# Kernel tuning notes

Hardware: AMD Instinct MI355X
Metric: run time of the kernel (lower is better)

The kernel has to match this reference:

```python
import jax, jax.numpy as jnp
import numpy as np

S, B, T, D, TS, V = 256, 8, 1024, 512, 512, 32000
LN_EPS = 1e-5


def setup_inputs() -> dict:
    key = jax.random.key(0)
    ks = jax.random.split(key, 16)
    std = 0.02
    inp = {
        "outs": jax.random.normal(ks[0], (S, B, D), jnp.float32),
        "graph_state": jax.random.normal(ks[1], (T, B, D), jnp.float32),
        "graph_padding_mask": jnp.zeros((B, T), bool),
        "copy_seq": jax.random.randint(ks[2], (T, B), 0, V),
        # single-head attention projections
        "Wq": std * jax.random.normal(ks[3], (D, D), jnp.float32),
        "bq": jnp.zeros((D,), jnp.float32),
        "Wk": std * jax.random.normal(ks[4], (D, D), jnp.float32),
        "bk": jnp.zeros((D,), jnp.float32),
        "Wv": std * jax.random.normal(ks[5], (D, D), jnp.float32),
        "bv": jnp.zeros((D,), jnp.float32),
        "Wo": std * jax.random.normal(ks[6], (D, D), jnp.float32),
        "bo": jnp.zeros((D,), jnp.float32),
        # layer norm
        "ln_g": jnp.ones((D,), jnp.float32),
        "ln_b": jnp.zeros((D,), jnp.float32),
        # transfer / generator / diverter linears
        "Wt": std * jax.random.normal(ks[7], (TS, D), jnp.float32),
        "bt": jnp.zeros((TS,), jnp.float32),
        "Wgen": std * jax.random.normal(ks[8], (V, TS), jnp.float32),
        "bgen": jnp.zeros((V,), jnp.float32),
        "Wdiv": std * jax.random.normal(ks[9], (2, TS), jnp.float32),
        "bdiv": jnp.zeros((2,), jnp.float32),
    }
    return inp


def _layer_norm(x, g, b):
    mu = jnp.mean(x, -1, keepdims=True)
    var = jnp.mean(jnp.square(x - mu), -1, keepdims=True)
    return (x - mu) * jax.lax.rsqrt(var + LN_EPS) * g + b


def reference(outs, graph_state, graph_padding_mask, copy_seq,
              Wq, bq, Wk, bk, Wv, bv, Wo, bo, ln_g, ln_b,
              Wt, bt, Wgen, bgen, Wdiv, bdiv):
    scale = 1.0 / jnp.sqrt(jnp.asarray(D, outs.dtype))
    q = (outs @ Wq.T + bq) * scale              # [S,B,D]
    k = graph_state @ Wk.T + bk                 # [T,B,D]
    v = graph_state @ Wv.T + bv                 # [T,B,D]
    scores = jnp.einsum("sbd,tbd->sbt", q, k)   # [S,B,T]
    scores = jnp.where(graph_padding_mask[None, :, :], -1e9, scores)
    attn = jax.nn.softmax(scores, axis=-1)      # alignment_weight [S,B,T]
    ctx = jnp.einsum("sbt,tbd->sbd", attn, v)
    x = ctx @ Wo.T + bo
    outs = _layer_norm(outs + x, ln_g, ln_b)
    outs_token = jnp.tanh(outs @ Wt.T + bt)     # [S,B,TS]
    gates = jax.nn.softmax(outs_token @ Wdiv.T + bdiv, axis=-1)
    gen_gate, copy_gate = gates[..., 0:1], gates[..., 1:2]
    probs = gen_gate * jax.nn.softmax(outs_token @ Wgen.T + bgen, axis=-1)  # [S,B,V]
    # copy indices: [T,B] -> [S,B,T] broadcast (indices < V, so no vocab extension)
    index = jnp.broadcast_to(copy_seq.T[None, :, :], (S, B, T))
    copy_probs = copy_gate * attn               # [S,B,T]
    s_idx = jnp.arange(S)[:, None, None]
    b_idx = jnp.arange(B)[None, :, None]
    probs = probs.at[s_idx, b_idx, index].add(copy_probs)
    ll = jnp.log(probs + 1e-12)
    return ll
```

## Files before the change

kernel.cpp:

```cpp
#include <hip/hip_runtime.h>
#include <hip/hip_bf16.h>
#include <math.h>

#define SS 256
#define BB 8
#define TT 1024
#define DD 512
#define TSD 512
#define VV 32000
#define LN_EPS_F 1e-5f
#define VHALF 16000

typedef __attribute__((ext_vector_type(8))) short bf16x8;
typedef __attribute__((ext_vector_type(4))) float f32x4;

__device__ __forceinline__ unsigned short f2bf(float f) {
    union { float f; unsigned int u; } c; c.f = f;
    unsigned int u = c.u;
    return (unsigned short)((u + 0x7fffu + ((u >> 16) & 1u)) >> 16);
}
__device__ __forceinline__ float bf2f(unsigned short s) {
    union { unsigned int u; float f; } c; c.u = ((unsigned int)s) << 16;
    return c.f;
}

__device__ __forceinline__ void glls16(const void* g, void* l) {
    __builtin_amdgcn_global_load_lds(
        (const __attribute__((address_space(1))) unsigned int*)g,
        (__attribute__((address_space(3))) unsigned int*)l,
        16, 0, 0);
}

__device__ __forceinline__ float warp_red_sum(float v) {
    for (int o = 32; o > 0; o >>= 1) v += __shfl_down(v, o, 64);
    return v;
}
__device__ __forceinline__ float warp_red_max(float v) {
    for (int o = 32; o > 0; o >>= 1) v = fmaxf(v, __shfl_down(v, o, 64));
    return v;
}
__device__ __forceinline__ float block_red_sum(float v, float* s) {
    int lane = threadIdx.x & 63, wid = threadIdx.x >> 6;
    v = warp_red_sum(v);
    __syncthreads();
    if (lane == 0) s[wid] = v;
    __syncthreads();
    float r = 0.f;
    int nw = blockDim.x >> 6;
    for (int i = 0; i < nw; i++) r += s[i];
    return r;
}
__device__ __forceinline__ float block_red_max(float v, float* s) {
    int lane = threadIdx.x & 63, wid = threadIdx.x >> 6;
    v = warp_red_max(v);
    __syncthreads();
    if (lane == 0) s[wid] = v;
    __syncthreads();
    float r = s[0];
    int nw = blockDim.x >> 6;
    for (int i = 1; i < nw; i++) r = fmaxf(r, s[i]);
    return r;
}

template<int IN_BF16, int OUT_BF16, int ACT, int SWZ>
__global__ __launch_bounds__(256) void mfma_gemm(
    const void* __restrict__ Ap, long long lda, long long aoff,
    const void* __restrict__ Bp, long long ldb, long long boff,
    const float* __restrict__ bias,
    void* __restrict__ Cp, long long ldc, long long coff,
    int K, float scale, float* __restrict__ rsum)
{
    __shared__ __align__(16) unsigned short smem[2 * 128 * 64];
    unsigned short* As = smem;
    unsigned short* Bs = smem + 128 * 64;
    const int tid = threadIdx.x;
    const int lane = tid & 63;
    const int wave = tid >> 6;
    const int wm = (wave >> 1) << 6;
    const int wn = (wave & 1) << 6;
    const int lane15 = lane & 15;
    const int quad = lane >> 4;

    int bx = blockIdx.x, by = blockIdx.y;
    if (SWZ) {
        unsigned int nx = gridDim.x;
        unsigned int nwg = nx * gridDim.y;
        unsigned int lin = blockIdx.y * nx + blockIdx.x;
        unsigned int q = nwg >> 3, r = nwg & 7u;
        unsigned int xcd = lin & 7u, loc = lin >> 3;
        unsigned int wg = (xcd < r ? xcd * (q + 1u) : r * (q + 1u) + (xcd - r) * q) + loc;
        bx = (int)(wg % nx);
        by = (int)(wg / nx);
    }
    const long long m0 = (long long)bx * 128;
    const long long n0 = (long long)by * 128;
    const long long z = blockIdx.z;

    f32x4 acc[4][4];
#pragma unroll
    for (int i = 0; i < 4; i++)
#pragma unroll
        for (int j = 0; j < 4; j++) acc[i][j] = (f32x4){0.f, 0.f, 0.f, 0.f};

    for (int k0 = 0; k0 < K; k0 += 64) {
        if (IN_BF16) {
            const unsigned short* A = (const unsigned short*)Ap + z * aoff;
            const unsigned short* B = (const unsigned short*)Bp + z * boff;
#pragma unroll
            for (int r = 0; r < 4; r++) {
                int c = r * 256 + tid;
                int row = c >> 3;
                int kc = (c & 7) ^ (row & 7);
                glls16(A + (m0 + row) * lda + k0 + kc * 8, &As[c * 8]);
                glls16(B + (n0 + row) * ldb + k0 + kc * 8, &Bs[c * 8]);
            }
        } else {
            const float* A = (const float*)Ap + z * aoff;
            const float* B = (const float*)Bp + z * boff;
#pragma unroll
            for (int r = 0; r < 4; r++) {
                int c = r * 256 + tid;
                int row = c >> 3;
                int kc = (c & 7) ^ (row & 7);
                const float* ga = A + (m0 + row) * lda + k0 + kc * 8;
                const float* gb = B + (n0 + row) * ldb + k0 + kc * 8;
                float4 a0 = *(const float4*)ga, a1 = *(const float4*)(ga + 4);
                float4 b0 = *(const float4*)gb, b1 = *(const float4*)(gb + 4);
                union { unsigned short us[8]; int4 v; } pa, pb;
                pa.us[0] = f2bf(a0.x); pa.us[1] = f2bf(a0.y); pa.us[2] = f2bf(a0.z); pa.us[3] = f2bf(a0.w);
                pa.us[4] = f2bf(a1.x); pa.us[5] = f2bf(a1.y); pa.us[6] = f2bf(a1.z); pa.us[7] = f2bf(a1.w);
                pb.us[0] = f2bf(b0.x); pb.us[1] = f2bf(b0.y); pb.us[2] = f2bf(b0.z); pb.us[3] = f2bf(b0.w);
                pb.us[4] = f2bf(b1.x); pb.us[5] = f2bf(b1.y); pb.us[6] = f2bf(b1.z); pb.us[7] = f2bf(b1.w);
                *(int4*)&As[c * 8] = pa.v;
                *(int4*)&Bs[c * 8] = pb.v;
            }
        }
        __syncthreads();
#pragma unroll
        for (int s = 0; s < 2; s++) {
            bf16x8 af[4], bfr[4];
#pragma unroll
            for (int i = 0; i < 4; i++) {
                int arow = wm + i * 16 + lane15;
                int kc = (s * 4 + quad) ^ (lane15 & 7);
                af[i] = *(const bf16x8*)&As[(arow * 8 + kc) * 8];
                int brow = wn + i * 16 + lane15;
                bfr[i] = *(const bf16x8*)&Bs[(brow * 8 + kc) * 8];
            }
#pragma unroll
            for (int i = 0; i < 4; i++)
#pragma unroll
                for (int j = 0; j < 4; j++)
                    acc[i][j] = __builtin_amdgcn_mfma_f32_16x16x32_bf16(af[i], bfr[j], acc[i][j], 0, 0, 0);
        }
        __syncthreads();
    }
    const long long zc = z * coff;
    float* sRowF = (float*)&smem[0];
    if (ACT == 2) {
        if (tid < 128) sRowF[tid] = 0.f;
        __syncthreads();
    }
#pragma unroll
    for (int i = 0; i < 4; i++) {
        float rs[4] = {0.f, 0.f, 0.f, 0.f};
#pragma unroll
        for (int j = 0; j < 4; j++) {
            float bv = bias ? bias[n0 + wn + j * 16 + lane15] : 0.f;
#pragma unroll
            for (int r2 = 0; r2 < 4; r2++) {
                float v = (acc[i][j][r2] + bv) * scale;
                if (ACT == 1) v = tanhf(v);
                if (ACT == 2) { v = __expf(v); rs[r2] += v; }
                acc[i][j][r2] = v;
            }
        }
        if (ACT == 2) {
#pragma unroll
            for (int r2 = 0; r2 < 4; r2++) {
                float s = rs[r2];
                s += __shfl_xor(s, 1, 64);
                s += __shfl_xor(s, 2, 64);
                s += __shfl_xor(s, 4, 64);
                s += __shfl_xor(s, 8, 64);
                if (lane15 == 0) atomicAdd(&sRowF[wm + i * 16 + quad * 4 + r2], s);
            }
        }
    }
    if (ACT == 2) {
        __syncthreads();
        if (tid < 128) atomicAdd(rsum + m0 + tid, sRowF[tid]);
        __syncthreads();
    }
    if (OUT_BF16) {
#pragma unroll
        for (int i = 0; i < 4; i++) {
#pragma unroll
            for (int r2 = 0; r2 < 4; r2++) {
                int lr = wm + i * 16 + quad * 4 + r2;
                int sw = (lr & 7) << 4;
#pragma unroll
                for (int j = 0; j < 4; j++) {
                    int lc = wn + j * 16 + lane15;
                    smem[lr * 128 + (lc ^ sw)] = f2bf(acc[i][j][r2]);
                }
            }
        }
        __syncthreads();
        unsigned short* Co = (unsigned short*)Cp + zc;
#pragma unroll
        for (int u = 0; u < 8; u++) {
            int e = tid + u * 256;
            int lr = e >> 4, lc8 = e & 15;
            int lcs = (lc8 * 8) ^ ((lr & 7) << 4);
            int4 vv4 = *(const int4*)&smem[lr * 128 + lcs];
            *(int4*)(Co + (m0 + lr) * ldc + n0 + lc8 * 8) = vv4;
        }
    } else {
#pragma unroll
        for (int i = 0; i < 4; i++) {
            long long rbase = m0 + wm + i * 16 + quad * 4;
#pragma unroll
            for (int j = 0; j < 4; j++) {
                long long col = n0 + wn + j * 16 + lane15;
#pragma unroll
                for (int r2 = 0; r2 < 4; r2++)
                    ((float*)Cp)[zc + (rbase + r2) * ldc + col] = acc[i][j][r2];
            }
        }
    }
}

__global__ __launch_bounds__(256) void attn_softmax(
    float* __restrict__ scores, unsigned short* __restrict__ scores_bf,
    const unsigned char* __restrict__ mask)
{
    __shared__ float red[4];
    int row = blockIdx.x;
    int b = row & (BB - 1);
    float* p = scores + (long long)row * TT;
    unsigned short* pb = scores_bf + (long long)row * TT;
    const unsigned char* mr = mask + (long long)b * TT;
    float vals[TT / 256];
    float lmax = -3.0e38f;
#pragma unroll
    for (int i = 0; i < TT / 256; i++) {
        int t = threadIdx.x + i * 256;
        float s = p[t];
        if (mr[t]) s = -1.0e9f;
        vals[i] = s;
        lmax = fmaxf(lmax, s);
    }
    float gmax = block_red_max(lmax, red);
    float lsum = 0.f;
#pragma unroll
    for (int i = 0; i < TT / 256; i++) {
        vals[i] = __expf(vals[i] - gmax);
        lsum += vals[i];
    }
    float gsum = block_red_sum(lsum, red);
    float inv = 1.f / gsum;
#pragma unroll
    for (int i = 0; i < TT / 256; i++) {
        float v = vals[i] * inv;
        int t = threadIdx.x + i * 256;
        p[t] = v;
        pb[t] = f2bf(v);
    }
}

__global__ __launch_bounds__(256) void transpose_v(
    const float* __restrict__ v, unsigned short* __restrict__ vT)
{
    __shared__ float tile[64][65];
    int b = blockIdx.z;
    int t0 = blockIdx.x * 64, d0 = blockIdx.y * 64;
    int tx = threadIdx.x & 63, ty = threadIdx.x >> 6;
#pragma unroll
    for (int i = ty; i < 64; i += 4)
        tile[i][tx] = v[((long long)(t0 + i) * BB + b) * DD + d0 + tx];
    __syncthreads();
#pragma unroll
    for (int i = ty; i < 64; i += 4)
        vT[((long long)b * DD + d0 + i) * TT + t0 + tx] = f2bf(tile[tx][i]);
}

__global__ __launch_bounds__(256) void add_ln(
    const float* __restrict__ outs, const float* __restrict__ xo,
    const float* __restrict__ g, const float* __restrict__ bln,
    float* __restrict__ y)
{
    __shared__ float red[4];
    int row = blockIdx.x;
    const float* o = outs + (long long)row * DD;
    const float* xp = xo + (long long)row * DD;
    float x[DD / 256];
    float s = 0.f;
#pragma unroll
    for (int i = 0; i < DD / 256; i++) {
        int d = threadIdx.x + i * 256;
        x[i] = o[d] + xp[d];
        s += x[i];
    }
    float mu = block_red_sum(s, red) * (1.f / DD);
    float s2 = 0.f;
#pragma unroll
    for (int i = 0; i < DD / 256; i++) {
        float dv = x[i] - mu;
        s2 += dv * dv;
    }
    float var = block_red_sum(s2, red) * (1.f / DD);
    float rinv = rsqrtf(var + LN_EPS_F);
#pragma unroll
    for (int i = 0; i < DD / 256; i++) {
        int d = threadIdx.x + i * 256;
        y[(long long)row * DD + d] = (x[i] - mu) * rinv * g[d] + bln[d];
    }
}

__global__ __launch_bounds__(256) void div_gates(
    const unsigned short* __restrict__ tok, const float* __restrict__ Wdiv,
    const float* __restrict__ bdiv, float* __restrict__ gen, float* __restrict__ cop)
{
    __shared__ float red[4];
    int row = blockIdx.x;
    const unsigned short* t = tok + (long long)row * TSD;
    float a0 = 0.f, a1 = 0.f;
#pragma unroll
    for (int i = 0; i < TSD / 256; i++) {
        int d = threadIdx.x + i * 256;
        float tv = bf2f(t[d]);
        a0 = fmaf(tv, Wdiv[d], a0);
        a1 = fmaf(tv, Wdiv[TSD + d], a1);
    }
    a0 = block_red_sum(a0, red);
    a1 = block_red_sum(a1, red);
    if (threadIdx.x == 0) {
        a0 += bdiv[0];
        a1 += bdiv[1];
        float m = fmaxf(a0, a1);
        float e0 = __expf(a0 - m), e1 = __expf(a1 - m);
        float inv = 1.f / (e0 + e1);
        gen[row] = e0 * inv;
        cop[row] = e1 * inv;
    }
}

__global__ __launch_bounds__(512) void copy_log_final(
    const unsigned short* __restrict__ eb, const float* __restrict__ attn,
    const float* __restrict__ cop, const float* __restrict__ gen,
    const float* __restrict__ gs, const int* __restrict__ seq,
    float* __restrict__ out)
{
    __shared__ __align__(16) float pc[VHALF];
    const int tid = threadIdx.x;
    const int row = blockIdx.x;
    const int half = blockIdx.y;
    const int base = half * VHALF;
    const int b = row & (BB - 1);

    for (int i = tid; i < VHALF; i += 512) pc[i] = 0.f;
    __syncthreads();

    const float cv = cop[row];
    const float* arow = attn + (long long)row * TT;
#pragma unroll
    for (int it = 0; it < 2; it++) {
        int t = tid + it * 512;
        int idx = seq[t * BB + b];
        int loc = idx - base;
        if (loc >= 0 && loc < VHALF)
            atomicAdd(&pc[loc], cv * arow[t]);
    }
    __syncthreads();

    const float ginv = gen[row] / gs[row];
    const unsigned short* erow = eb + (long long)row * VV + base;
    float* orow = out + (long long)row * VV + base;
    const float4* pc4 = (const float4*)pc;
    for (int c = tid; c < VHALF / 8; c += 512) {
        bf16x8 ev = *(const bf16x8*)(erow + c * 8);
        float4 p0 = pc4[c * 2], p1 = pc4[c * 2 + 1];
        float4 o0, o1;
        o0.x = __logf(fmaf(bf2f((unsigned short)ev[0]), ginv, p0.x) + 1e-12f);
        o0.y = __logf(fmaf(bf2f((unsigned short)ev[1]), ginv, p0.y) + 1e-12f);
        o0.z = __logf(fmaf(bf2f((unsigned short)ev[2]), ginv, p0.z) + 1e-12f);
        o0.w = __logf(fmaf(bf2f((unsigned short)ev[3]), ginv, p0.w) + 1e-12f);
        o1.x = __logf(fmaf(bf2f((unsigned short)ev[4]), ginv, p1.x) + 1e-12f);
        o1.y = __logf(fmaf(bf2f((unsigned short)ev[5]), ginv, p1.y) + 1e-12f);
        o1.z = __logf(fmaf(bf2f((unsigned short)ev[6]), ginv, p1.z) + 1e-12f);
        o1.w = __logf(fmaf(bf2f((unsigned short)ev[7]), ginv, p1.w) + 1e-12f);
        ((float4*)orow)[c * 2] = o0;
        ((float4*)orow)[c * 2 + 1] = o1;
    }
}

__global__ __launch_bounds__(256) void cast_f32_bf16(
    const float* __restrict__ in, unsigned short* __restrict__ o, long long n8,
    float* __restrict__ gszero)
{
    long long i = (long long)blockIdx.x * 256 + threadIdx.x;
    if (gszero && blockIdx.x < 8) gszero[blockIdx.x * 256 + threadIdx.x] = 0.f;
    if (i >= n8) return;
    const float4* p = (const float4*)in + i * 2;
    float4 a = p[0], b = p[1];
    union { unsigned short us[8]; int4 v; } pk;
    pk.us[0] = f2bf(a.x); pk.us[1] = f2bf(a.y); pk.us[2] = f2bf(a.z); pk.us[3] = f2bf(a.w);
    pk.us[4] = f2bf(b.x); pk.us[5] = f2bf(b.y); pk.us[6] = f2bf(b.z); pk.us[7] = f2bf(b.w);
    ((int4*)o)[i] = pk.v;
}

extern "C" void kernel_launch(void* const* d_in, const int* in_sizes, int n_in,
                              void* d_out, int out_size, void* d_ws, size_t ws_size,
                              hipStream_t stream)
{
    const float* outs = (const float*)d_in[0];
    const float* gstate = (const float*)d_in[1];
    const unsigned char* mask = (const unsigned char*)d_in[2];
    const int* seq = (const int*)d_in[3];
    const float* Wq = (const float*)d_in[4];  const float* bq = (const float*)d_in[5];
    const float* Wk = (const float*)d_in[6];  const float* bk = (const float*)d_in[7];
    const float* Wv = (const float*)d_in[8];  const float* bv = (const float*)d_in[9];
    const float* Wo = (const float*)d_in[10]; const float* bo = (const float*)d_in[11];
    const float* lng = (const float*)d_in[12]; const float* lnb = (const float*)d_in[13];
    const float* Wt = (const float*)d_in[14]; const float* bt = (const float*)d_in[15];
    const float* Wgen = (const float*)d_in[16]; const float* bgen = (const float*)d_in[17];
    const float* Wdiv = (const float*)d_in[18]; const float* bdiv = (const float*)d_in[19];
    float* out = (float*)d_out;

    char* w = (char*)d_ws;
    unsigned short* qb    = (unsigned short*)w; w += 2048LL * 512 * 2;
    unsigned short* kb    = (unsigned short*)w; w += 8192LL * 512 * 2;
    unsigned short* tokb  = (unsigned short*)w; w += 2048LL * 512 * 2;
    unsigned short* wgenb = (unsigned short*)w; w += 32000LL * 512 * 2;
    unsigned short* vTb   = (unsigned short*)w; w += 8LL * 512 * 1024 * 2;
    unsigned short* attnb = (unsigned short*)w; w += 2048LL * 1024 * 2;
    unsigned short* eb    = (unsigned short*)w; w += 2048LL * 32000 * 2;
    float* vv   = (float*)w; w += 8192LL * 512 * 4;
    float* attn = (float*)w; w += 2048LL * 1024 * 4;
    float* ctx  = (float*)w; w += 2048LL * 512 * 4;
    float* xo   = (float*)w; w += 2048LL * 512 * 4;
    float* y    = (float*)w; w += 2048LL * 512 * 4;
    float* gen  = (float*)w; w += 2048 * 4;
    float* cop  = (float*)w; w += 2048 * 4;
    float* gs   = (float*)w; w += 2048 * 4;

    float qscale = 1.0f / sqrtf((float)DD);
    dim3 blk(256);

    cast_f32_bf16<<<8000, blk, 0, stream>>>(Wgen, wgenb, 32000LL * 512 / 8, gs);

    mfma_gemm<0, 1, 0, 0><<<dim3(16, 4, 1), blk, 0, stream>>>(outs, 512, 0, Wq, 512, 0, bq, qb, 512, 0, 512, qscale, nullptr);
    mfma_gemm<0, 1, 0, 0><<<dim3(64, 4, 1), blk, 0, stream>>>(gstate, 512, 0, Wk, 512, 0, bk, kb, 512, 0, 512, 1.f, nullptr);
    mfma_gemm<0, 0, 0, 0><<<dim3(64, 4, 1), blk, 0, stream>>>(gstate, 512, 0, Wv, 512, 0, bv, vv, 512, 0, 512, 1.f, nullptr);
    transpose_v<<<dim3(16, 8, 8), blk, 0, stream>>>(vv, vTb);
    mfma_gemm<1, 0, 0, 0><<<dim3(2, 8, 8), blk, 0, stream>>>(qb, 4096, 512, kb, 4096, 512, nullptr, attn, 8192, 1024, 512, 1.f, nullptr);
    attn_softmax<<<2048, blk, 0, stream>>>(attn, attnb, mask);
    mfma_gemm<1, 0, 0, 0><<<dim3(2, 4, 8), blk, 0, stream>>>(attnb, 8192, 1024, vTb, 1024, 524288, nullptr, ctx, 4096, 512, 1024, 1.f, nullptr);
    mfma_gemm<0, 0, 0, 0><<<dim3(16, 4, 1), blk, 0, stream>>>(ctx, 512, 0, Wo, 512, 0, bo, xo, 512, 0, 512, 1.f, nullptr);
    add_ln<<<2048, blk, 0, stream>>>(outs, xo, lng, lnb, y);
    mfma_gemm<0, 1, 1, 0><<<dim3(16, 4, 1), blk, 0, stream>>>(y, 512, 0, Wt, 512, 0, bt, tokb, 512, 0, 512, 1.f, nullptr);
    div_gates<<<2048, blk, 0, stream>>>(tokb, Wdiv, bdiv, gen, cop);
    mfma_gemm<1, 1, 2, 1><<<dim3(16, 250, 1), blk, 0, stream>>>(tokb, 512, 0, wgenb, 512, 0, bgen, eb, 32000, 0, 512, 1.f, gs);
    copy_log_final<<<dim3(2048, 2), dim3(512), 0, stream>>>(eb, attn, cop, gen, gs, seq, out);
}
```

Before: 756.9 us.

## Add dedicated 256x256-tile generator GEMM with fused exp and row-sum epilogue

Replaces the generic GEMM launch for the vocabulary projection (2048x32000x512) with a specialized kernel. It uses 512-thread blocks, 256x256 output tiles, double-buffered LDS loads with direct global-to-LDS copies, and a swizzled workgroup ordering meant to improve L2 reuse of the weight matrix. The exp-plus-bias and row-sum reduction are fused into the epilogue, which writes bf16 output through swizzled LDS. Larger tiles reduce operand re-reads, at the cost of more registers per thread (acc[8][4]) and a full 64KB of LDS, which may lower occupancy.

```diff
diff --git a/kernel.cpp b/kernel.cpp
--- a/kernel.cpp
+++ b/kernel.cpp
@@ -228,6 +228,150 @@
                     ((float*)Cp)[zc + (rbase + r2) * ldc + col] = acc[i][j][r2];
             }
         }
+    }
+}
+
+__global__ __launch_bounds__(512) void mfma_gemm_big(
+    const unsigned short* __restrict__ A,
+    const unsigned short* __restrict__ B,
+    const float* __restrict__ bias,
+    unsigned short* __restrict__ C,
+    float* __restrict__ rsum)
+{
+    __shared__ __align__(16) unsigned short smem[32768];
+    const int tid = threadIdx.x;
+    const int lane = tid & 63;
+    const int wave = tid >> 6;
+    const int lane15 = lane & 15;
+    const int quad = lane >> 4;
+    const int wm = (wave >> 2) << 7;
+    const int wn = (wave & 3) << 6;
+
+    unsigned int lin = blockIdx.y * 8u + blockIdx.x;
+    unsigned int wg = (lin & 7u) * 125u + (lin >> 3);
+    const long long m0 = (long long)(wg & 7u) * 256;
+    const long long n0 = (long long)(wg >> 3) * 256;
+
+    f32x4 acc[8][4];
+#pragma unroll
+    for (int i = 0; i < 8; i++)
+#pragma unroll
+        for (int j = 0; j < 4; j++) acc[i][j] = (f32x4){0.f, 0.f, 0.f, 0.f};
+
+#define STAGE_BIG(kt, buf)                                                        \
+    {                                                                             \
+        const int k0s = (kt) << 5;                                                \
+        unsigned short* Asb = &smem[(buf) * 8192];                                \
+        unsigned short* Bsb = &smem[16384 + (buf) * 8192];                        \
+        _Pragma("unroll")                                                         \
+        for (int r = 0; r < 2; r++) {                                             \
+            int c = r * 512 + tid;                                                \
+            int row = c >> 2;                                                     \
+            int kc = (c & 3) ^ (row & 3);                                         \
+            glls16(A + (m0 + row) * 512 + k0s + kc * 8, &Asb[c * 8]);             \
+            glls16(B + (n0 + row) * 512 + k0s + kc * 8, &Bsb[c * 8]);             \
+        }                                                                         \
+    }
+
+    STAGE_BIG(0, 0)
+    STAGE_BIG(1, 1)
+    asm volatile("s_waitcnt vmcnt(4)" ::: "memory");
+    __builtin_amdgcn_s_barrier();
+
+    for (int kt = 0; kt < 16; kt++) {
+        const int buf = kt & 1;
+        const unsigned short* Asb = &smem[buf * 8192];
+        const unsigned short* Bsb = &smem[16384 + buf * 8192];
+        const int kcp = quad ^ (lane15 & 3);
+        bf16x8 bfr[4];
+#pragma unroll
+        for (int j = 0; j < 4; j++) {
+            int brow = wn + j * 16 + lane15;
+            bfr[j] = *(const bf16x8*)&Bsb[(brow * 4 + kcp) * 8];
+        }
+#pragma unroll
+        for (int ih = 0; ih < 2; ih++) {
+            bf16x8 af[4];
+#pragma unroll
+            for (int i2 = 0; i2 < 4; i2++) {
+                int arow = wm + (ih * 4 + i2) * 16 + lane15;
+                af[i2] = *(const bf16x8*)&Asb[(arow * 4 + kcp) * 8];
+            }
+            __builtin_amdgcn_s_setprio(1);
+#pragma unroll
+            for (int i2 = 0; i2 < 4; i2++)
+#pragma unroll
+                for (int j = 0; j < 4; j++)
+                    acc[ih * 4 + i2][j] = __builtin_amdgcn_mfma_f32_16x16x32_bf16(
+                        af[i2], bfr[j], acc[ih * 4 + i2][j], 0, 0, 0);
+            __builtin_amdgcn_s_setprio(0);
+        }
+        __builtin_amdgcn_s_barrier();
+        if (kt < 14) {
+            STAGE_BIG(kt + 2, buf)
+            asm volatile("s_waitcnt vmcnt(4)" ::: "memory");
+        } else {
+            asm volatile("s_waitcnt vmcnt(0)" ::: "memory");
+        }
+        __builtin_amdgcn_s_barrier();
+    }
+#undef STAGE_BIG
+
+    float* sRowF = (float*)smem;
+    if (tid < 256) sRowF[tid] = 0.f;
+    __syncthreads();
+#pragma unroll
+    for (int i = 0; i < 8; i++) {
+        float rs[4] = {0.f, 0.f, 0.f, 0.f};
+#pragma unroll
+        for (int j = 0; j < 4; j++) {
+            float bv = bias[n0 + wn + j * 16 + lane15];
+#pragma unroll
+            for (int r2 = 0; r2 < 4; r2++) {
+                float v = __expf(acc[i][j][r2] + bv);
+                acc[i][j][r2] = v;
+                rs[r2] += v;
+            }
+        }
+#pragma unroll
+        for (int r2 = 0; r2 < 4; r2++) {
+            float s = rs[r2];
+            s += __shfl_xor(s, 1, 64);
+            s += __shfl_xor(s, 2, 64);
+            s += __shfl_xor(s, 4, 64);
+            s += __shfl_xor(s, 8, 64);
+            if (lane15 == 0) atomicAdd(&sRowF[wm + i * 16 + quad * 4 + r2], s);
+        }
+    }
+    __syncthreads();
+    if (tid < 256) atomicAdd(rsum + m0 + tid, sRowF[tid]);
+    __syncthreads();
+#pragma unroll
+    for (int h = 0; h < 2; h++) {
+        if ((wave >> 2) == h) {
+#pragma unroll
+            for (int i = 0; i < 8; i++)
+#pragma unroll
+                for (int r2 = 0; r2 < 4; r2++) {
+                    int lrl = i * 16 + quad * 4 + r2;
+                    int sw = (lrl & 7) << 4;
+#pragma unroll
+                    for (int j = 0; j < 4; j++) {
+                        int lc = wn + j * 16 + lane15;
+                        smem[lrl * 256 + (lc ^ sw)] = f2bf(acc[i][j][r2]);
+                    }
+                }
+        }
+        __syncthreads();
+#pragma unroll
+        for (int u = 0; u < 8; u++) {
+            int e = tid + u * 512;
+            int lrl = e >> 5, ch = e & 31;
+            int lcs = (ch * 8) ^ ((lrl & 7) << 4);
+            int4 vv4 = *(const int4*)&smem[lrl * 256 + lcs];
+            *(int4*)(C + (m0 + h * 128 + lrl) * 32000LL + n0 + ch * 8) = vv4;
+        }
+        __syncthreads();
     }
 }
 
@@ -461,6 +605,6 @@
     add_ln<<<2048, blk, 0, stream>>>(outs, xo, lng, lnb, y);
     mfma_gemm<0, 1, 1, 0><<<dim3(16, 4, 1), blk, 0, stream>>>(y, 512, 0, Wt, 512, 0, bt, tokb, 512, 0, 512, 1.f, nullptr);
     div_gates<<<2048, blk, 0, stream>>>(tokb, Wdiv, bdiv, gen, cop);
-    mfma_gemm<1, 1, 2, 1><<<dim3(16, 250, 1), blk, 0, stream>>>(tokb, 512, 0, wgenb, 512, 0, bgen, eb, 32000, 0, 512, 1.f, gs);
+    mfma_gemm_big<<<dim3(8, 125), dim3(512), 0, stream>>>(tokb, wgenb, bgen, eb, gs);
     copy_log_final<<<dim3(2048, 2), dim3(512), 0, stream>>>(eb, attn, cop, gen, gs, seq, out);
 }
```

Measured after the change: 772.6 us. 1.02x slower.

## Fuse QKV projections and Wgen cast into one launch; fold V transpose and gates

Applied to the files above, without the earlier changes.

Merges the Q, K and V projection GEMMs and the Wgen bf16 cast into a single multi-role kernel dispatched by block index. The V GEMM now writes a transposed bf16 layout directly from shared memory, which removes the fp32 V buffer and the separate transpose kernel. The diverter gate computation moves into the final copy/log kernel, so the div_gates launch and its gen/cop buffers are gone. This saves launch overhead and intermediate memory traffic. In exchange, gates are recomputed per vocab half, and the fused kernel mixes heterogeneous block roles, which can unbalance the work across blocks.

```diff
diff --git a/kernel.cpp b/kernel.cpp
--- a/kernel.cpp
+++ b/kernel.cpp
@@ -62,15 +62,15 @@
     return r;
 }
 
-template<int IN_BF16, int OUT_BF16, int ACT, int SWZ>
-__global__ __launch_bounds__(256) void mfma_gemm(
+template<int IN_BF16, int OUT_MODE, int ACT>
+__device__ __forceinline__ void gemm_body(
+    unsigned short* smem, int bx, int by, int z,
     const void* __restrict__ Ap, long long lda, long long aoff,
     const void* __restrict__ Bp, long long ldb, long long boff,
     const float* __restrict__ bias,
     void* __restrict__ Cp, long long ldc, long long coff,
     int K, float scale, float* __restrict__ rsum)
 {
-    __shared__ __align__(16) unsigned short smem[2 * 128 * 64];
     unsigned short* As = smem;
     unsigned short* Bs = smem + 128 * 64;
     const int tid = threadIdx.x;
@@ -80,21 +80,8 @@
     const int wn = (wave & 1) << 6;
     const int lane15 = lane & 15;
     const int quad = lane >> 4;
-
-    int bx = blockIdx.x, by = blockIdx.y;
-    if (SWZ) {
-        unsigned int nx = gridDim.x;
-        unsigned int nwg = nx * gridDim.y;
-        unsigned int lin = blockIdx.y * nx + blockIdx.x;
-        unsigned int q = nwg >> 3, r = nwg & 7u;
-        unsigned int xcd = lin & 7u, loc = lin >> 3;
-        unsigned int wg = (xcd < r ? xcd * (q + 1u) : r * (q + 1u) + (xcd - r) * q) + loc;
-        bx = (int)(wg % nx);
-        by = (int)(wg / nx);
-    }
     const long long m0 = (long long)bx * 128;
     const long long n0 = (long long)by * 128;
-    const long long z = blockIdx.z;
 
     f32x4 acc[4][4];
 #pragma unroll
@@ -192,7 +179,7 @@
         if (tid < 128) atomicAdd(rsum + m0 + tid, sRowF[tid]);
         __syncthreads();
     }
-    if (OUT_BF16) {
+    if (OUT_MODE >= 1) {
 #pragma unroll
         for (int i = 0; i < 4; i++) {
 #pragma unroll
@@ -207,15 +194,34 @@
             }
         }
         __syncthreads();
-        unsigned short* Co = (unsigned short*)Cp + zc;
-#pragma unroll
-        for (int u = 0; u < 8; u++) {
-            int e = tid + u * 256;
-            int lr = e >> 4, lc8 = e & 15;
-            int lcs = (lc8 * 8) ^ ((lr & 7) << 4);
-            int4 vv4 = *(const int4*)&smem[lr * 128 + lcs];
-            *(int4*)(Co + (m0 + lr) * ldc + n0 + lc8 * 8) = vv4;
-        }
+        if (OUT_MODE == 1) {
+            unsigned short* Co = (unsigned short*)Cp + zc;
+#pragma unroll
+            for (int u = 0; u < 8; u++) {
+                int e = tid + u * 256;
+                int lr = e >> 4, lc8 = e & 15;
+                int lcs = (lc8 * 8) ^ ((lr & 7) << 4);
+                int4 vv4 = *(const int4*)&smem[lr * 128 + lcs];
+                *(int4*)(Co + (m0 + lr) * ldc + n0 + lc8 * 8) = vv4;
+            }
+        } else {
+            unsigned short* vT = (unsigned short*)Cp;
+            const int t0g = (int)(m0 >> 3);
+#pragma unroll
+            for (int u = 0; u < 4; u++) {
+                int e = tid + u * 256;
+                int b = e >> 7, dl = e & 127;
+                int sw = (b & 7) << 4;
+                union { unsigned short us[16]; int4 v[2]; } pk;
+#pragma unroll
+                for (int tl = 0; tl < 16; tl++)
+                    pk.us[tl] = smem[(tl * 8 + b) * 128 + (dl ^ sw)];
+                unsigned short* dst = vT + (long long)b * (DD * TT) + (long long)(n0 + dl) * TT + t0g;
+                *(int4*)dst = pk.v[0];
+                *(int4*)(dst + 8) = pk.v[1];
+            }
+        }
+        __syncthreads();
     } else {
 #pragma unroll
         for (int i = 0; i < 4; i++) {
@@ -228,6 +234,65 @@
                     ((float*)Cp)[zc + (rbase + r2) * ldc + col] = acc[i][j][r2];
             }
         }
+    }
+}
+
+template<int IN_BF16, int OUT_MODE, int ACT, int SWZ>
+__global__ __launch_bounds__(256) void mfma_gemm(
+    const void* __restrict__ Ap, long long lda, long long aoff,
+    const void* __restrict__ Bp, long long ldb, long long boff,
+    const float* __restrict__ bias,
+    void* __restrict__ Cp, long long ldc, long long coff,
+    int K, float scale, float* __restrict__ rsum)
+{
+    __shared__ __align__(16) unsigned short smem[2 * 128 * 64];
+    int bx = blockIdx.x, by = blockIdx.y;
+    if (SWZ) {
+        unsigned int nx = gridDim.x;
+        unsigned int nwg = nx * gridDim.y;
+        unsigned int lin = blockIdx.y * nx + blockIdx.x;
+        unsigned int q = nwg >> 3, r = nwg & 7u;
+        unsigned int xcd = lin & 7u, loc = lin >> 3;
+        unsigned int wg = (xcd < r ? xcd * (q + 1u) : r * (q + 1u) + (xcd - r) * q) + loc;
+        bx = (int)(wg % nx);
+        by = (int)(wg / nx);
+    }
+    gemm_body<IN_BF16, OUT_MODE, ACT>(smem, bx, by, blockIdx.z,
+        Ap, lda, aoff, Bp, ldb, boff, bias, Cp, ldc, coff, K, scale, rsum);
+}
+
+__global__ __launch_bounds__(256) void front_fused(
+    const float* __restrict__ outs, const float* __restrict__ Wq, const float* __restrict__ bq,
+    const float* __restrict__ gstate, const float* __restrict__ Wk, const float* __restrict__ bk,
+    const float* __restrict__ Wv, const float* __restrict__ bv,
+    unsigned short* __restrict__ qb, unsigned short* __restrict__ kb,
+    unsigned short* __restrict__ vTb,
+    const float* __restrict__ Wgen, unsigned short* __restrict__ wgenb,
+    float* __restrict__ gs, float qscale)
+{
+    extern __shared__ __align__(16) unsigned short dsm[];
+    const int bid = blockIdx.x;
+    if (bid < 64) {
+        gemm_body<0, 1, 0>(dsm, bid & 15, bid >> 4, 0,
+            outs, 512, 0, Wq, 512, 0, bq, qb, 512, 0, 512, qscale, nullptr);
+    } else if (bid < 320) {
+        int lb = bid - 64;
+        gemm_body<0, 1, 0>(dsm, lb & 63, lb >> 6, 0,
+            gstate, 512, 0, Wk, 512, 0, bk, kb, 512, 0, 512, 1.f, nullptr);
+    } else if (bid < 576) {
+        int lb = bid - 320;
+        gemm_body<0, 2, 0>(dsm, lb & 63, lb >> 6, 0,
+            gstate, 512, 0, Wv, 512, 0, bv, vTb, 0, 0, 512, 1.f, nullptr);
+    } else {
+        int lb = bid - 576;
+        if (lb < 8) gs[lb * 256 + threadIdx.x] = 0.f;
+        long long i = (long long)lb * 256 + threadIdx.x;
+        const float4* p = (const float4*)Wgen + i * 2;
+        float4 a = p[0], b = p[1];
+        union { unsigned short us[8]; int4 v; } pk;
+        pk.us[0] = f2bf(a.x); pk.us[1] = f2bf(a.y); pk.us[2] = f2bf(a.z); pk.us[3] = f2bf(a.w);
+        pk.us[4] = f2bf(b.x); pk.us[5] = f2bf(b.y); pk.us[6] = f2bf(b.z); pk.us[7] = f2bf(b.w);
+        ((int4*)wgenb)[i] = pk.v;
     }
 }
 
@@ -269,22 +334,6 @@
     }
 }
 
-__global__ __launch_bounds__(256) void transpose_v(
-    const float* __restrict__ v, unsigned short* __restrict__ vT)
-{
-    __shared__ float tile[64][65];
-    int b = blockIdx.z;
-    int t0 = blockIdx.x * 64, d0 = blockIdx.y * 64;
-    int tx = threadIdx.x & 63, ty = threadIdx.x >> 6;
-#pragma unroll
-    for (int i = ty; i < 64; i += 4)
-        tile[i][tx] = v[((long long)(t0 + i) * BB + b) * DD + d0 + tx];
-    __syncthreads();
-#pragma unroll
-    for (int i = ty; i < 64; i += 4)
-        vT[((long long)b * DD + d0 + i) * TT + t0 + tx] = f2bf(tile[tx][i]);
-}
-
 __global__ __launch_bounds__(256) void add_ln(
     const float* __restrict__ outs, const float* __restrict__ xo,
     const float* __restrict__ g, const float* __restrict__ bln,
@@ -318,41 +367,14 @@
     }
 }
 
-__global__ __launch_bounds__(256) void div_gates(
-    const unsigned short* __restrict__ tok, const float* __restrict__ Wdiv,
-    const float* __restrict__ bdiv, float* __restrict__ gen, float* __restrict__ cop)
-{
-    __shared__ float red[4];
-    int row = blockIdx.x;
-    const unsigned short* t = tok + (long long)row * TSD;
-    float a0 = 0.f, a1 = 0.f;
-#pragma unroll
-    for (int i = 0; i < TSD / 256; i++) {
-        int d = threadIdx.x + i * 256;
-        float tv = bf2f(t[d]);
-        a0 = fmaf(tv, Wdiv[d], a0);
-        a1 = fmaf(tv, Wdiv[TSD + d], a1);
-    }
-    a0 = block_red_sum(a0, red);
-    a1 = block_red_sum(a1, red);
-    if (threadIdx.x == 0) {
-        a0 += bdiv[0];
-        a1 += bdiv[1];
-        float m = fmaxf(a0, a1);
-        float e0 = __expf(a0 - m), e1 = __expf(a1 - m);
-        float inv = 1.f / (e0 + e1);
-        gen[row] = e0 * inv;
-        cop[row] = e1 * inv;
-    }
-}
-
 __global__ __launch_bounds__(512) void copy_log_final(
     const unsigned short* __restrict__ eb, const float* __restrict__ attn,
-    const float* __restrict__ cop, const float* __restrict__ gen,
-    const float* __restrict__ gs, const int* __restrict__ seq,
-    float* __restrict__ out)
+    const unsigned short* __restrict__ tok, const float* __restrict__ Wdiv,
+    const float* __restrict__ bdiv, const float* __restrict__ gs,
+    const int* __restrict__ seq, float* __restrict__ out)
 {
     __shared__ __align__(16) float pc[VHALF];
+    __shared__ float red[8];
     const int tid = threadIdx.x;
     const int row = blockIdx.x;
     const int half = blockIdx.y;
@@ -360,9 +382,21 @@
     const int b = row & (BB - 1);
 
     for (int i = tid; i < VHALF; i += 512) pc[i] = 0.f;
-    __syncthreads();
-
-    const float cv = cop[row];
+
+    float tv = bf2f(tok[(long long)row * TSD + tid]);
+    float a0 = tv * Wdiv[tid];
+    float a1 = tv * Wdiv[TSD + tid];
+    a0 = block_red_sum(a0, red);
+    a1 = block_red_sum(a1, red);
+    a0 += bdiv[0];
+    a1 += bdiv[1];
+    float mx = fmaxf(a0, a1);
+    float e0 = __expf(a0 - mx), e1 = __expf(a1 - mx);
+    float inv2 = 1.f / (e0 + e1);
+    const float cv = e1 * inv2;
+    const float ginv = (e0 * inv2) / gs[row];
+    __syncthreads();
+
     const float* arow = attn + (long long)row * TT;
 #pragma unroll
     for (int it = 0; it < 2; it++) {
@@ -374,7 +408,6 @@
     }
     __syncthreads();
 
-    const float ginv = gen[row] / gs[row];
     const unsigned short* erow = eb + (long long)row * VV + base;
     float* orow = out + (long long)row * VV + base;
     const float4* pc4 = (const float4*)pc;
@@ -395,21 +428,6 @@
     }
 }
 
-__global__ __launch_bounds__(256) void cast_f32_bf16(
-    const float* __restrict__ in, unsigned short* __restrict__ o, long long n8,
-    float* __restrict__ gszero)
-{
-    long long i = (long long)blockIdx.x * 256 + threadIdx.x;
-    if (gszero && blockIdx.x < 8) gszero[blockIdx.x * 256 + threadIdx.x] = 0.f;
-    if (i >= n8) return;
-    const float4* p = (const float4*)in + i * 2;
-    float4 a = p[0], b = p[1];
-    union { unsigned short us[8]; int4 v; } pk;
-    pk.us[0] = f2bf(a.x); pk.us[1] = f2bf(a.y); pk.us[2] = f2bf(a.z); pk.us[3] = f2bf(a.w);
-    pk.us[4] = f2bf(b.x); pk.us[5] = f2bf(b.y); pk.us[6] = f2bf(b.z); pk.us[7] = f2bf(b.w);
-    ((int4*)o)[i] = pk.v;
-}
-
 extern "C" void kernel_launch(void* const* d_in, const int* in_sizes, int n_in,
                               void* d_out, int out_size, void* d_ws, size_t ws_size,
                               hipStream_t stream)
@@ -436,31 +454,23 @@
     unsigned short* vTb   = (unsigned short*)w; w += 8LL * 512 * 1024 * 2;
     unsigned short* attnb = (unsigned short*)w; w += 2048LL * 1024 * 2;
     unsigned short* eb    = (unsigned short*)w; w += 2048LL * 32000 * 2;
-    float* vv   = (float*)w; w += 8192LL * 512 * 4;
     float* attn = (float*)w; w += 2048LL * 1024 * 4;
     float* ctx  = (float*)w; w += 2048LL * 512 * 4;
     float* xo   = (float*)w; w += 2048LL * 512 * 4;
     float* y    = (float*)w; w += 2048LL * 512 * 4;
-    float* gen  = (float*)w; w += 2048 * 4;
-    float* cop  = (float*)w; w += 2048 * 4;
     float* gs   = (float*)w; w += 2048 * 4;
 
     float qscale = 1.0f / sqrtf((float)DD);
     dim3 blk(256);
 
-    cast_f32_bf16<<<8000, blk, 0, stream>>>(Wgen, wgenb, 32000LL * 512 / 8, gs);
-
-    mfma_gemm<0, 1, 0, 0><<<dim3(16, 4, 1), blk, 0, stream>>>(outs, 512, 0, Wq, 512, 0, bq, qb, 512, 0, 512, qscale, nullptr);
-    mfma_gemm<0, 1, 0, 0><<<dim3(64, 4, 1), blk, 0, stream>>>(gstate, 512, 0, Wk, 512, 0, bk, kb, 512, 0, 512, 1.f, nullptr);
-    mfma_gemm<0, 0, 0, 0><<<dim3(64, 4, 1), blk, 0, stream>>>(gstate, 512, 0, Wv, 512, 0, bv, vv, 512, 0, 512, 1.f, nullptr);
-    transpose_v<<<dim3(16, 8, 8), blk, 0, stream>>>(vv, vTb);
+    front_fused<<<8576, blk, 32768, stream>>>(outs, Wq, bq, gstate, Wk, bk, Wv, bv,
+                                              qb, kb, vTb, Wgen, wgenb, gs, qscale);
     mfma_gemm<1, 0, 0, 0><<<dim3(2, 8, 8), blk, 0, stream>>>(qb, 4096, 512, kb, 4096, 512, nullptr, attn, 8192, 1024, 512, 1.f, nullptr);
     attn_softmax<<<2048, blk, 0, stream>>>(attn, attnb, mask);
     mfma_gemm<1, 0, 0, 0><<<dim3(2, 4, 8), blk, 0, stream>>>(attnb, 8192, 1024, vTb, 1024, 524288, nullptr, ctx, 4096, 512, 1024, 1.f, nullptr);
     mfma_gemm<0, 0, 0, 0><<<dim3(16, 4, 1), blk, 0, stream>>>(ctx, 512, 0, Wo, 512, 0, bo, xo, 512, 0, 512, 1.f, nullptr);
     add_ln<<<2048, blk, 0, stream>>>(outs, xo, lng, lnb, y);
     mfma_gemm<0, 1, 1, 0><<<dim3(16, 4, 1), blk, 0, stream>>>(y, 512, 0, Wt, 512, 0, bt, tokb, 512, 0, 512, 1.f, nullptr);
-    div_gates<<<2048, blk, 0, stream>>>(tokb, Wdiv, bdiv, gen, cop);
     mfma_gemm<1, 1, 2, 1><<<dim3(16, 250, 1), blk, 0, stream>>>(tokb, 512, 0, wgenb, 512, 0, bgen, eb, 32000, 0, 512, 1.f, gs);
-    copy_log_final<<<dim3(2048, 2), dim3(512), 0, stream>>>(eb, attn, cop, gen, gs, seq, out);
-}
+    copy_log_final<<<dim3(2048, 2), dim3(512), 0, stream>>>(eb, attn, tokb, Wdiv, bdiv, gs, seq, out);
+}
```

Measured after the change: 702.3 us. -7.2%, faster.
